# Kernel tuning notes

Measured on AMD Instinct MI355X. Metric: run time of the kernel, lower is better.

The kernel has to match this reference:

```python
import jax, jax.numpy as jnp
import numpy as np

H = 32  # hidden size, fixed by the source module


def setup_inputs() -> dict:
    key = jax.random.key(0)
    ks = jax.random.split(key, 11)
    B, T = 1024, 999
    s = 0.1  # weight init scale
    return {
        "input": jax.random.normal(ks[0], (B, T), jnp.float32),
        "W_ih1": jax.random.normal(ks[1], (4 * H, 1), jnp.float32) * s,
        "W_hh1": jax.random.normal(ks[2], (4 * H, H), jnp.float32) * s,
        "b_ih1": jax.random.normal(ks[3], (4 * H,), jnp.float32) * s,
        "b_hh1": jax.random.normal(ks[4], (4 * H,), jnp.float32) * s,
        "W_ih2": jax.random.normal(ks[5], (4 * H, H), jnp.float32) * s,
        "W_hh2": jax.random.normal(ks[6], (4 * H, H), jnp.float32) * s,
        "b_ih2": jax.random.normal(ks[7], (4 * H,), jnp.float32) * s,
        "b_hh2": jax.random.normal(ks[8], (4 * H,), jnp.float32) * s,
        "W_lin": jax.random.normal(ks[9], (1, H), jnp.float32) * s,
        "b_lin": jax.random.normal(ks[10], (1,), jnp.float32) * s,
        "future": 1000,
    }


def _lstm_cell(x, h, c, W_ih, W_hh, b_ih, b_hh):
    # PyTorch LSTMCell: gates = x@W_ih^T + b_ih + h@W_hh^T + b_hh, order i,f,g,o
    z = x @ W_ih.T + h @ W_hh.T + (b_ih + b_hh)
    i, f, g, o = jnp.split(z, 4, axis=-1)
    c_new = jax.nn.sigmoid(f) * c + jax.nn.sigmoid(i) * jnp.tanh(g)
    h_new = jax.nn.sigmoid(o) * jnp.tanh(c_new)
    return h_new, c_new


def reference(input, W_ih1, W_hh1, b_ih1, b_hh1, W_ih2, W_hh2, b_ih2, b_hh2,
              W_lin, b_lin, future):
    B = input.shape[0]
    dt = input.dtype
    z = jnp.zeros((B, H), dt)

    def step_tf(carry, x_t):  # teacher-forced phase, x_t: [B]
        h1, c1, h2, c2 = carry
        h1, c1 = _lstm_cell(x_t[:, None], h1, c1, W_ih1, W_hh1, b_ih1, b_hh1)
        h2, c2 = _lstm_cell(h1, h2, c2, W_ih2, W_hh2, b_ih2, b_hh2)
        out = h2 @ W_lin.T + b_lin  # [B,1]
        return (h1, c1, h2, c2), out[:, 0]

    carry, outs1 = jax.lax.scan(step_tf, (z, z, z, z), input.T)  # outs1: [T,B]

    def step_gen(carry, _):
        h1, c1, h2, c2, out = carry
        h1, c1 = _lstm_cell(out, h1, c1, W_ih1, W_hh1, b_ih1, b_hh1)
        h2, c2 = _lstm_cell(h1, h2, c2, W_ih2, W_hh2, b_ih2, b_hh2)
        out = h2 @ W_lin.T + b_lin
        return (h1, c1, h2, c2, out), out[:, 0]

    last_out = outs1[-1][:, None]
    _, outs2 = jax.lax.scan(step_gen, (*carry, last_out), None, length=future)

    return jnp.concatenate([outs1, outs2], axis=0).T  # [B, T+future]
```

## Files before the change

kernel.cpp:

```cpp
#include <hip/hip_runtime.h>

#define HH 32
#define LOG2E 1.44269504088896340736f
#define KCH 16

typedef float v2f __attribute__((ext_vector_type(2)));

#define DPPF(v, ctrl) \
    __int_as_float(__builtin_amdgcn_update_dpp(0, __float_as_int(v), (ctrl), 0xF, 0xF, true))
#define QP_B0 0x00
#define QP_B1 0x55
#define QP_B2 0xAA
#define QP_B3 0xFF
#define DPP_ROR4  0x124
#define DPP_ROR8  0x128
#define SWZ(v, pat) __int_as_float(__builtin_amdgcn_ds_swizzle(__float_as_int(v), (pat)))

__device__ __forceinline__ float hw_exp2(float x) {
    float r; asm("v_exp_f32 %0, %1" : "=v"(r) : "v"(x)); return r;
}
__device__ __forceinline__ float sigm_e(float z, float e) {
    return __builtin_amdgcn_rcpf(1.0f + hw_exp2(z * e));
}
__device__ __forceinline__ v2f pk_fma(v2f a, v2f b, v2f c) {
    return __builtin_elementwise_fma(a, b, c);
}
__device__ __forceinline__ void load_bc(const float* p, v2f* d) {
#pragma unroll
    for (int r = 0; r < 8; ++r) {
        float4 v = ((const float4*)p)[r];
        d[2*r]   = (v2f){v.x, v.y};
        d[2*r+1] = (v2f){v.z, v.w};
    }
}
__device__ __forceinline__ float out_reduce(float p) {
    p += DPPF(p, DPP_ROR4);
    p += DPPF(p, DPP_ROR8);
    p += SWZ(p, 0x401F);
    p += __shfl_xor(p, 32, 64);
    return p;
}

template<bool ACC>
__device__ __forceinline__ void dot2(const v2f* hv, const v2f* mA, const v2f* mB,
                                     v2f& P0, v2f& P1, v2f& P2, v2f& P3) {
    if (ACC) {
        P0 = pk_fma(hv[0], mA[0], P0); P1 = pk_fma(hv[1], mA[1], P1);
        P2 = pk_fma(hv[0], mB[0], P2); P3 = pk_fma(hv[1], mB[1], P3);
    } else {
        P0 = hv[0] * mA[0]; P1 = hv[1] * mA[1];
        P2 = hv[0] * mB[0]; P3 = hv[1] * mB[1];
    }
#pragma unroll
    for (int r = 2; r < 16; r += 2) {
        P0 = pk_fma(hv[r],   mA[r],   P0);
        P1 = pk_fma(hv[r+1], mA[r+1], P1);
        P2 = pk_fma(hv[r],   mB[r],   P2);
        P3 = pk_fma(hv[r+1], mB[r+1], P3);
    }
}

__device__ __forceinline__ void gate_hc(float zA, float zB, float es, float mm, float cc,
                                        float& cA, float& cB, float& hA, float& hB) {
    float acA = fmaf(mm, sigm_e(zA, es), cc);
    float acB = fmaf(mm, sigm_e(zB, es), cc);
    float iA = DPPF(acA, QP_B0), fA = DPPF(acA, QP_B1);
    float gA = DPPF(acA, QP_B2), oA = DPPF(acA, QP_B3);
    float iB = DPPF(acB, QP_B0), fB = DPPF(acB, QP_B1);
    float gB = DPPF(acB, QP_B2), oB = DPPF(acB, QP_B3);
    cA = fmaf(fA, cA, iA * gA);
    cB = fmaf(fB, cB, iB * gB);
    hA = oA * fmaf(2.0f, sigm_e(cA, -2.0f * LOG2E), -1.0f);
    hB = oB * fmaf(2.0f, sigm_e(cB, -2.0f * LOG2E), -1.0f);
}

__global__ __launch_bounds__(128, 2)
void lstm_seq_kernel(const float* __restrict__ input,
                     const float* __restrict__ W_ih1, const float* __restrict__ W_hh1,
                     const float* __restrict__ b_ih1, const float* __restrict__ b_hh1,
                     const float* __restrict__ W_ih2, const float* __restrict__ W_hh2,
                     const float* __restrict__ b_ih2, const float* __restrict__ b_hh2,
                     const float* __restrict__ W_lin, const float* __restrict__ b_lin,
                     float* __restrict__ out, int T, int total)
{
    const int b    = blockIdx.x;
    const int tid  = threadIdx.x;
    const int w    = tid >> 6;
    const int lane = tid & 63;
    const int q    = lane & 3;
    const int ch   = lane >> 2;
    const int rowA = (q << 5) | ch;
    const int rowB = (q << 5) | (ch + 16);

    __shared__ __align__(16) float ring[2 * KCH * HH];
    __shared__ __align__(16) float h1x[HH];
    __shared__ __align__(16) float h2s[HH];

    const bool  isg = (q == 2);
    const float es  = isg ? (-2.0f * LOG2E) : (-LOG2E);
    const float mm  = isg ? 2.0f : 1.0f;
    const float cc  = isg ? -1.0f : 0.0f;

    v2f m1A[16], m1B[16], m2A[16], m2B[16], wl[16];
    float wxA = 0.f, wxB = 0.f, bA, bB, wlA = 0.f, wlB = 0.f, blin;
    if (w == 0) {
        const v2f* pA = (const v2f*)(W_hh1 + rowA * HH);
        const v2f* pB = (const v2f*)(W_hh1 + rowB * HH);
        const v2f* wp = (const v2f*)W_lin;
#pragma unroll
        for (int r = 0; r < 16; ++r) { m1A[r] = pA[r]; m1B[r] = pB[r]; wl[r] = wp[r]; }
        wxA = W_ih1[rowA]; wxB = W_ih1[rowB];
        bA  = b_ih1[rowA] + b_hh1[rowA];
        bB  = b_ih1[rowB] + b_hh1[rowB];
    } else {
        const v2f* pA = (const v2f*)(W_ih2 + rowA * HH);
        const v2f* pB = (const v2f*)(W_ih2 + rowB * HH);
        const v2f* qA = (const v2f*)(W_hh2 + rowA * HH);
        const v2f* qB = (const v2f*)(W_hh2 + rowB * HH);
#pragma unroll
        for (int r = 0; r < 16; ++r) { m1A[r] = pA[r]; m1B[r] = pB[r];
                                       m2A[r] = qA[r]; m2B[r] = qB[r]; }
        bA  = b_ih2[rowA] + b_hh2[rowA];
        bB  = b_ih2[rowB] + b_hh2[rowB];
        wlA = W_lin[ch]; wlB = W_lin[ch + 16];
    }
    blin = b_lin[0];

    float cA = 0.f, cB = 0.f;
    v2f p0 = {0.f,0.f}, p1 = {0.f,0.f}, p2 = {0.f,0.f}, p3 = {0.f,0.f};

    const float* __restrict__ inp  = input + (size_t)b * T;
    float* __restrict__       outp = out   + (size_t)b * total;

    if (w == 0) {
        int t = 0;
        float xcur = inp[0];
        for (int cb = 0; t < T; ++cb) {
            float* buf = ring + (cb & 1) * (KCH * HH);
            int S = T - t; if (S > KCH) S = KCH;
            for (int s = 0; s < S; ++s, ++t) {
                float x = xcur;
                int tn = t + 1;
                xcur = inp[tn < T ? tn : 0];
                float z1A = fmaf(x, wxA, bA + (p0.x + p0.y) + (p1.x + p1.y));
                float z1B = fmaf(x, wxB, bB + (p2.x + p2.y) + (p3.x + p3.y));
                float hA, hB;
                gate_hc(z1A, z1B, es, mm, cc, cA, cB, hA, hB);
                float* slot = buf + s * HH;
                if (q == 0) { slot[ch] = hA; slot[ch + 16] = hB; }
                v2f hv[16]; load_bc(slot, hv);
                dot2<false>(hv, m1A, m1B, p0, p1, p2, p3);
            }
            __syncthreads();
        }
        __syncthreads();
    } else {
        __syncthreads();
        int t = 0;
        for (int cb = 0; t < T; ++cb) {
            const float* buf = ring + (cb & 1) * (KCH * HH);
            int S = T - t; if (S > KCH) S = KCH;
            for (int s = 0; s < S; ++s, ++t) {
                v2f hv[16]; load_bc(buf + s * HH, hv);
                dot2<true>(hv, m1A, m1B, p0, p1, p2, p3);
                float z2A = bA + (p0.x + p0.y) + (p1.x + p1.y);
                float z2B = bB + (p2.x + p2.y) + (p3.x + p3.y);
                float hA, hB;
                gate_hc(z2A, z2B, es, mm, cc, cA, cB, hA, hB);
                if (q == 0) { h2s[ch] = hA; h2s[ch + 16] = hB; }
                v2f gv[16]; load_bc(h2s, gv);
                dot2<false>(gv, m2A, m2B, p0, p1, p2, p3);
                float pr = fmaf(hA, wlA, hB * wlB);
                float ov = out_reduce(pr) + blin;
                if (lane == 0) outp[t] = ov;
            }
            __syncthreads();
        }
    }

    for (int t = T; t < total; ++t) {
        __syncthreads();
        if (w == 0) {
            v2f gv[16]; load_bc(h2s, gv);
            v2f oa = gv[0] * wl[0], ob = gv[1] * wl[1];
#pragma unroll
            for (int r = 2; r < 16; r += 2) { oa = pk_fma(gv[r],   wl[r],   oa);
                                              ob = pk_fma(gv[r+1], wl[r+1], ob); }
            float xo = (oa.x + oa.y) + (ob.x + ob.y) + blin;
            if (t > T && lane == 0) outp[t - 1] = xo;
            float z1A = fmaf(xo, wxA, bA + (p0.x + p0.y) + (p1.x + p1.y));
            float z1B = fmaf(xo, wxB, bB + (p2.x + p2.y) + (p3.x + p3.y));
            float hA, hB;
            gate_hc(z1A, z1B, es, mm, cc, cA, cB, hA, hB);
            if (q == 0) { h1x[ch] = hA; h1x[ch + 16] = hB; }
        } else {
            v2f gv[16]; load_bc(h2s, gv);
            dot2<false>(gv, m2A, m2B, p0, p1, p2, p3);
        }
        __syncthreads();
        if (w == 0) {
            v2f hv[16]; load_bc(h1x, hv);
            dot2<false>(hv, m1A, m1B, p0, p1, p2, p3);
        } else {
            v2f hv[16]; load_bc(h1x, hv);
            dot2<true>(hv, m1A, m1B, p0, p1, p2, p3);
            float z2A = bA + (p0.x + p0.y) + (p1.x + p1.y);
            float z2B = bB + (p2.x + p2.y) + (p3.x + p3.y);
            float hA, hB;
            gate_hc(z2A, z2B, es, mm, cc, cA, cB, hA, hB);
            if (q == 0) { h2s[ch] = hA; h2s[ch + 16] = hB; }
        }
    }
    __syncthreads();
    if (w == 0) {
        v2f gv[16]; load_bc(h2s, gv);
        v2f oa = gv[0] * wl[0], ob = gv[1] * wl[1];
#pragma unroll
        for (int r = 2; r < 16; r += 2) { oa = pk_fma(gv[r],   wl[r],   oa);
                                          ob = pk_fma(gv[r+1], wl[r+1], ob); }
        if (lane == 0) outp[total - 1] = (oa.x + oa.y) + (ob.x + ob.y) + blin;
    }
}

extern "C" void kernel_launch(void* const* d_in, const int* in_sizes, int n_in,
                              void* d_out, int out_size, void* d_ws, size_t ws_size,
                              hipStream_t stream) {
    const int B = 1024;
    const int T = in_sizes[0] / B;
    const int total = out_size / B;

    lstm_seq_kernel<<<dim3(B), dim3(128), 0, stream>>>(
        (const float*)d_in[0],
        (const float*)d_in[1], (const float*)d_in[2],
        (const float*)d_in[3], (const float*)d_in[4],
        (const float*)d_in[5], (const float*)d_in[6],
        (const float*)d_in[7], (const float*)d_in[8],
        (const float*)d_in[9], (const float*)d_in[10],
        (float*)d_out, T, total);
}
```

Before: 1.205 ms.

## Split each LSTM cell across two waves and pipeline layers with per-step barriers

Each block now uses four waves: two per LSTM layer, each wave owning 16 hidden channels, replacing one wave per layer that handled 32 channels each. The teacher-forced phase drops the decoupled 16-step ring buffer and instead runs layer 1 one step ahead of layer 2 in lockstep, with double-buffered hidden states in shared memory and a block barrier every step. The output projection is reduced across the two layer-2 waves through shared memory. The aim is to halve the per-wave dot-product and gate work on the serial critical path, at the cost of a __syncthreads on every timestep and twice the threads per block.

```diff
diff --git a/kernel.cpp b/kernel.cpp
--- a/kernel.cpp
+++ b/kernel.cpp
@@ -2,7 +2,6 @@
 
 #define HH 32
 #define LOG2E 1.44269504088896340736f
-#define KCH 16
 
 typedef float v2f __attribute__((ext_vector_type(2)));
 
@@ -25,14 +24,7 @@
 __device__ __forceinline__ v2f pk_fma(v2f a, v2f b, v2f c) {
     return __builtin_elementwise_fma(a, b, c);
 }
-__device__ __forceinline__ void load_bc(const float* p, v2f* d) {
-#pragma unroll
-    for (int r = 0; r < 8; ++r) {
-        float4 v = ((const float4*)p)[r];
-        d[2*r]   = (v2f){v.x, v.y};
-        d[2*r+1] = (v2f){v.z, v.w};
-    }
-}
+
 __device__ __forceinline__ float out_reduce(float p) {
     p += DPPF(p, DPP_ROR4);
     p += DPPF(p, DPP_ROR8);
@@ -41,40 +33,51 @@
     return p;
 }
 
-template<bool ACC>
-__device__ __forceinline__ void dot2(const v2f* hv, const v2f* mA, const v2f* mB,
-                                     v2f& P0, v2f& P1, v2f& P2, v2f& P3) {
-    if (ACC) {
-        P0 = pk_fma(hv[0], mA[0], P0); P1 = pk_fma(hv[1], mA[1], P1);
-        P2 = pk_fma(hv[0], mB[0], P2); P3 = pk_fma(hv[1], mB[1], P3);
-    } else {
-        P0 = hv[0] * mA[0]; P1 = hv[1] * mA[1];
-        P2 = hv[0] * mB[0]; P3 = hv[1] * mB[1];
-    }
+__device__ __forceinline__ float dotv(const float* va, const v2f* m) {
+    const float4* pa = (const float4*)va;
+    float4 a = pa[0], b = pa[1];
+    v2f s0 = (v2f){a.x,a.y} * m[0], s1 = (v2f){a.z,a.w} * m[1];
+    v2f s2 = (v2f){b.x,b.y} * m[2], s3 = (v2f){b.z,b.w} * m[3];
 #pragma unroll
-    for (int r = 2; r < 16; r += 2) {
-        P0 = pk_fma(hv[r],   mA[r],   P0);
-        P1 = pk_fma(hv[r+1], mA[r+1], P1);
-        P2 = pk_fma(hv[r],   mB[r],   P2);
-        P3 = pk_fma(hv[r+1], mB[r+1], P3);
-    }
-}
-
-__device__ __forceinline__ void gate_hc(float zA, float zB, float es, float mm, float cc,
-                                        float& cA, float& cB, float& hA, float& hB) {
-    float acA = fmaf(mm, sigm_e(zA, es), cc);
-    float acB = fmaf(mm, sigm_e(zB, es), cc);
-    float iA = DPPF(acA, QP_B0), fA = DPPF(acA, QP_B1);
-    float gA = DPPF(acA, QP_B2), oA = DPPF(acA, QP_B3);
-    float iB = DPPF(acB, QP_B0), fB = DPPF(acB, QP_B1);
-    float gB = DPPF(acB, QP_B2), oB = DPPF(acB, QP_B3);
-    cA = fmaf(fA, cA, iA * gA);
-    cB = fmaf(fB, cB, iB * gB);
-    hA = oA * fmaf(2.0f, sigm_e(cA, -2.0f * LOG2E), -1.0f);
-    hB = oB * fmaf(2.0f, sigm_e(cB, -2.0f * LOG2E), -1.0f);
-}
-
-__global__ __launch_bounds__(128, 2)
+    for (int rr = 2; rr < 8; rr += 2) {
+        float4 c = pa[rr], d = pa[rr+1];
+        s0 = pk_fma((v2f){c.x,c.y}, m[2*rr],   s0);
+        s1 = pk_fma((v2f){c.z,c.w}, m[2*rr+1], s1);
+        s2 = pk_fma((v2f){d.x,d.y}, m[2*rr+2], s2);
+        s3 = pk_fma((v2f){d.z,d.w}, m[2*rr+3], s3);
+    }
+    v2f t = (s0 + s1) + (s2 + s3);
+    return t.x + t.y;
+}
+
+__device__ __forceinline__ float dotv2f(const float* va, const v2f* ma,
+                                        const float* vb, const v2f* mb) {
+    const float4* pa = (const float4*)va;
+    const float4* pb = (const float4*)vb;
+    float4 a = pa[0], b = pb[0];
+    v2f s0 = (v2f){a.x,a.y} * ma[0], s1 = (v2f){a.z,a.w} * ma[1];
+    v2f s2 = (v2f){b.x,b.y} * mb[0], s3 = (v2f){b.z,b.w} * mb[1];
+#pragma unroll
+    for (int rr = 1; rr < 8; ++rr) {
+        float4 c = pa[rr], d = pb[rr];
+        s0 = pk_fma((v2f){c.x,c.y}, ma[2*rr],   s0);
+        s1 = pk_fma((v2f){c.z,c.w}, ma[2*rr+1], s1);
+        s2 = pk_fma((v2f){d.x,d.y}, mb[2*rr],   s2);
+        s3 = pk_fma((v2f){d.z,d.w}, mb[2*rr+1], s3);
+    }
+    v2f t = (s0 + s1) + (s2 + s3);
+    return t.x + t.y;
+}
+
+__device__ __forceinline__ float gate1(float z, float es, float mm, float cc, float& c) {
+    float ac = fmaf(mm, sigm_e(z, es), cc);
+    float gi = DPPF(ac, QP_B0), gf = DPPF(ac, QP_B1);
+    float gg = DPPF(ac, QP_B2), go = DPPF(ac, QP_B3);
+    c = fmaf(gf, c, gi * gg);
+    return go * fmaf(2.0f, sigm_e(c, -2.0f * LOG2E), -1.0f);
+}
+
+__global__ __launch_bounds__(256, 4)
 void lstm_seq_kernel(const float* __restrict__ input,
                      const float* __restrict__ W_ih1, const float* __restrict__ W_hh1,
                      const float* __restrict__ b_ih1, const float* __restrict__ b_hh1,
@@ -85,140 +88,105 @@
 {
     const int b    = blockIdx.x;
     const int tid  = threadIdx.x;
-    const int w    = tid >> 6;
+    const int wv   = tid >> 6;
     const int lane = tid & 63;
+    const int cell = wv >> 1;
+    const int half = wv & 1;
     const int q    = lane & 3;
-    const int ch   = lane >> 2;
-    const int rowA = (q << 5) | ch;
-    const int rowB = (q << 5) | (ch + 16);
-
-    __shared__ __align__(16) float ring[2 * KCH * HH];
-    __shared__ __align__(16) float h1x[HH];
-    __shared__ __align__(16) float h2s[HH];
+    const int ch   = (lane >> 2) + (half << 4);
+    const int row  = (q << 5) | ch;
+
+    __shared__ __align__(16) float h1buf[2][HH];
+    __shared__ __align__(16) float h2buf[2][HH];
+    __shared__ float outP[2][2];
+
+    if (tid < HH) {
+        h1buf[0][tid] = 0.f; h1buf[1][tid] = 0.f;
+        h2buf[0][tid] = 0.f; h2buf[1][tid] = 0.f;
+    }
+    if (tid < 4) outP[tid >> 1][tid & 1] = 0.f;
 
     const bool  isg = (q == 2);
     const float es  = isg ? (-2.0f * LOG2E) : (-LOG2E);
     const float mm  = isg ? 2.0f : 1.0f;
     const float cc  = isg ? -1.0f : 0.0f;
 
-    v2f m1A[16], m1B[16], m2A[16], m2B[16], wl[16];
-    float wxA = 0.f, wxB = 0.f, bA, bB, wlA = 0.f, wlB = 0.f, blin;
-    if (w == 0) {
-        const v2f* pA = (const v2f*)(W_hh1 + rowA * HH);
-        const v2f* pB = (const v2f*)(W_hh1 + rowB * HH);
-        const v2f* wp = (const v2f*)W_lin;
+    const v2f* m1p = (const v2f*)((cell == 0 ? W_hh1 : W_ih2) + row * HH);
+    const v2f* m2p = (cell == 0) ? (const v2f*)W_lin
+                                 : (const v2f*)(W_hh2 + row * HH);
+    v2f m1[16], m2[16];
 #pragma unroll
-        for (int r = 0; r < 16; ++r) { m1A[r] = pA[r]; m1B[r] = pB[r]; wl[r] = wp[r]; }
-        wxA = W_ih1[rowA]; wxB = W_ih1[rowB];
-        bA  = b_ih1[rowA] + b_hh1[rowA];
-        bB  = b_ih1[rowB] + b_hh1[rowB];
-    } else {
-        const v2f* pA = (const v2f*)(W_ih2 + rowA * HH);
-        const v2f* pB = (const v2f*)(W_ih2 + rowB * HH);
-        const v2f* qA = (const v2f*)(W_hh2 + rowA * HH);
-        const v2f* qB = (const v2f*)(W_hh2 + rowB * HH);
-#pragma unroll
-        for (int r = 0; r < 16; ++r) { m1A[r] = pA[r]; m1B[r] = pB[r];
-                                       m2A[r] = qA[r]; m2B[r] = qB[r]; }
-        bA  = b_ih2[rowA] + b_hh2[rowA];
-        bB  = b_ih2[rowB] + b_hh2[rowB];
-        wlA = W_lin[ch]; wlB = W_lin[ch + 16];
-    }
-    blin = b_lin[0];
-
-    float cA = 0.f, cB = 0.f;
-    v2f p0 = {0.f,0.f}, p1 = {0.f,0.f}, p2 = {0.f,0.f}, p3 = {0.f,0.f};
+    for (int r = 0; r < 16; ++r) { m1[r] = m1p[r]; m2[r] = m2p[r]; }
+
+    const float wx  = W_ih1[row];
+    const float bb  = (cell == 0) ? (b_ih1[row] + b_hh1[row])
+                                  : (b_ih2[row] + b_hh2[row]);
+    const float wlc = W_lin[ch];
+    const float blin = b_lin[0];
+
+    float cst = 0.f;
+    float pAR = 0.f;
 
     const float* __restrict__ inp  = input + (size_t)b * T;
     float* __restrict__       outp = out   + (size_t)b * total;
 
-    if (w == 0) {
-        int t = 0;
-        float xcur = inp[0];
-        for (int cb = 0; t < T; ++cb) {
-            float* buf = ring + (cb & 1) * (KCH * HH);
-            int S = T - t; if (S > KCH) S = KCH;
-            for (int s = 0; s < S; ++s, ++t) {
+    float xcur = inp[0];
+    for (int t = 0; t <= T; ++t) {
+        __syncthreads();
+        if (cell == 0) {
+            if (t < T) {
+                float pd = dotv(h1buf[(t + 1) & 1], m1);
                 float x = xcur;
                 int tn = t + 1;
                 xcur = inp[tn < T ? tn : 0];
-                float z1A = fmaf(x, wxA, bA + (p0.x + p0.y) + (p1.x + p1.y));
-                float z1B = fmaf(x, wxB, bB + (p2.x + p2.y) + (p3.x + p3.y));
-                float hA, hB;
-                gate_hc(z1A, z1B, es, mm, cc, cA, cB, hA, hB);
-                float* slot = buf + s * HH;
-                if (q == 0) { slot[ch] = hA; slot[ch + 16] = hB; }
-                v2f hv[16]; load_bc(slot, hv);
-                dot2<false>(hv, m1A, m1B, p0, p1, p2, p3);
+                float z1 = fmaf(x, wx, bb + pd);
+                float h = gate1(z1, es, mm, cc, cst);
+                if (q == 0) h1buf[t & 1][ch] = h;
+            } else {
+                pAR = dotv(h1buf[(T - 1) & 1], m1);
             }
-            __syncthreads();
+        } else {
+            if (t >= 1) {
+                float zd = dotv2f(h1buf[(t - 1) & 1], m1, h2buf[t & 1], m2);
+                float z2 = bb + zd;
+                float h = gate1(z2, es, mm, cc, cst);
+                if (q == 0) h2buf[(t - 1) & 1][ch] = h;
+                float po = out_reduce(h * wlc);
+                if (lane == 0) outP[(t - 1) & 1][half] = po;
+            }
+            if (t >= 2 && wv == 2 && lane == 0)
+                outp[t - 2] = outP[t & 1][0] + outP[t & 1][1] + blin;
+        }
+    }
+
+    float* h2x = h2buf[(T - 1) & 1];
+    float* h1x = h1buf[0];
+    float sAR = 0.f;
+
+    for (int t = T; t < total; ++t) {
+        __syncthreads();
+        if (cell == 0) {
+            float xo = dotv(h2x, m2) + blin;
+            if (wv == 0 && lane == 0) outp[t - 1] = xo;
+            float z1 = fmaf(xo, wx, bb + pAR);
+            float h = gate1(z1, es, mm, cc, cst);
+            if (q == 0) h1x[ch] = h;
+        } else {
+            sAR = dotv(h2x, m2);
         }
         __syncthreads();
-    } else {
-        __syncthreads();
-        int t = 0;
-        for (int cb = 0; t < T; ++cb) {
-            const float* buf = ring + (cb & 1) * (KCH * HH);
-            int S = T - t; if (S > KCH) S = KCH;
-            for (int s = 0; s < S; ++s, ++t) {
-                v2f hv[16]; load_bc(buf + s * HH, hv);
-                dot2<true>(hv, m1A, m1B, p0, p1, p2, p3);
-                float z2A = bA + (p0.x + p0.y) + (p1.x + p1.y);
-                float z2B = bB + (p2.x + p2.y) + (p3.x + p3.y);
-                float hA, hB;
-                gate_hc(z2A, z2B, es, mm, cc, cA, cB, hA, hB);
-                if (q == 0) { h2s[ch] = hA; h2s[ch + 16] = hB; }
-                v2f gv[16]; load_bc(h2s, gv);
-                dot2<false>(gv, m2A, m2B, p0, p1, p2, p3);
-                float pr = fmaf(hA, wlA, hB * wlB);
-                float ov = out_reduce(pr) + blin;
-                if (lane == 0) outp[t] = ov;
-            }
-            __syncthreads();
+        if (cell == 0) {
+            pAR = dotv(h1x, m1);
+        } else {
+            float z2 = bb + sAR + dotv(h1x, m1);
+            float h = gate1(z2, es, mm, cc, cst);
+            if (q == 0) h2x[ch] = h;
         }
     }
-
-    for (int t = T; t < total; ++t) {
-        __syncthreads();
-        if (w == 0) {
-            v2f gv[16]; load_bc(h2s, gv);
-            v2f oa = gv[0] * wl[0], ob = gv[1] * wl[1];
-#pragma unroll
-            for (int r = 2; r < 16; r += 2) { oa = pk_fma(gv[r],   wl[r],   oa);
-                                              ob = pk_fma(gv[r+1], wl[r+1], ob); }
-            float xo = (oa.x + oa.y) + (ob.x + ob.y) + blin;
-            if (t > T && lane == 0) outp[t - 1] = xo;
-            float z1A = fmaf(xo, wxA, bA + (p0.x + p0.y) + (p1.x + p1.y));
-            float z1B = fmaf(xo, wxB, bB + (p2.x + p2.y) + (p3.x + p3.y));
-            float hA, hB;
-            gate_hc(z1A, z1B, es, mm, cc, cA, cB, hA, hB);
-            if (q == 0) { h1x[ch] = hA; h1x[ch + 16] = hB; }
-        } else {
-            v2f gv[16]; load_bc(h2s, gv);
-            dot2<false>(gv, m2A, m2B, p0, p1, p2, p3);
-        }
-        __syncthreads();
-        if (w == 0) {
-            v2f hv[16]; load_bc(h1x, hv);
-            dot2<false>(hv, m1A, m1B, p0, p1, p2, p3);
-        } else {
-            v2f hv[16]; load_bc(h1x, hv);
-            dot2<true>(hv, m1A, m1B, p0, p1, p2, p3);
-            float z2A = bA + (p0.x + p0.y) + (p1.x + p1.y);
-            float z2B = bB + (p2.x + p2.y) + (p3.x + p3.y);
-            float hA, hB;
-            gate_hc(z2A, z2B, es, mm, cc, cA, cB, hA, hB);
-            if (q == 0) { h2s[ch] = hA; h2s[ch + 16] = hB; }
-        }
-    }
     __syncthreads();
-    if (w == 0) {
-        v2f gv[16]; load_bc(h2s, gv);
-        v2f oa = gv[0] * wl[0], ob = gv[1] * wl[1];
-#pragma unroll
-        for (int r = 2; r < 16; r += 2) { oa = pk_fma(gv[r],   wl[r],   oa);
-                                          ob = pk_fma(gv[r+1], wl[r+1], ob); }
-        if (lane == 0) outp[total - 1] = (oa.x + oa.y) + (ob.x + ob.y) + blin;
+    if (wv == 0) {
+        float xo = dotv(h2x, m2) + blin;
+        if (lane == 0) outp[total - 1] = xo;
     }
 }
 
@@ -229,7 +197,7 @@
     const int T = in_sizes[0] / B;
     const int total = out_size / B;
 
-    lstm_seq_kernel<<<dim3(B), dim3(128), 0, stream>>>(
+    lstm_seq_kernel<<<dim3(B), dim3(256), 0, stream>>>(
         (const float*)d_in[0],
         (const float*)d_in[1], (const float*)d_in[2],
         (const float*)d_in[3], (const float*)d_in[4],
```

After: 1.403 ms. 1.16x slower.

## Run autoregressive phase on a single wavefront without block barriers

Applied to the files above, without the earlier changes.

After the teacher-forced phase, wave 1 saves its layer-2 cell state to shared memory and exits, and wave 0 runs both LSTM layers alone for the generation steps. This removes the two __syncthreads per step and the cross-wave handoff. W_ih2 and W_hh2 are loaded into registers and W_hh1 is moved to padded shared memory to limit register pressure. The cost is serialising work that two waves previously shared, and adding LDS reads for the W_hh1 dot product.

```diff
diff --git a/kernel.cpp b/kernel.cpp
--- a/kernel.cpp
+++ b/kernel.cpp
@@ -3,6 +3,7 @@
 #define HH 32
 #define LOG2E 1.44269504088896340736f
 #define KCH 16
+#define WPAD 36
 
 typedef float v2f __attribute__((ext_vector_type(2)));
 
@@ -95,6 +96,8 @@
     __shared__ __align__(16) float ring[2 * KCH * HH];
     __shared__ __align__(16) float h1x[HH];
     __shared__ __align__(16) float h2s[HH];
+    __shared__ __align__(16) float c2x[HH];
+    __shared__ __align__(16) float whh1l[128 * WPAD];
 
     const bool  isg = (q == 2);
     const float es  = isg ? (-2.0f * LOG2E) : (-LOG2E);
@@ -174,45 +177,68 @@
                 float ov = out_reduce(pr) + blin;
                 if (lane == 0) outp[t] = ov;
             }
+            if (t >= T && q == 0) { c2x[ch] = cA; c2x[ch + 16] = cB; }
             __syncthreads();
         }
-    }
+        return;
+    }
+
+#pragma unroll
+    for (int k = 0; k < 16; ++k) {
+        ((v2f*)(whh1l + rowA * WPAD))[k] = m1A[k];
+        ((v2f*)(whh1l + rowB * WPAD))[k] = m1B[k];
+    }
+    float c2A = c2x[ch], c2B = c2x[ch + 16];
+    v2f i2A[16], i2B[16], w2A[16], w2B[16];
+    {
+        const v2f* a1 = (const v2f*)(W_ih2 + rowA * HH);
+        const v2f* a2 = (const v2f*)(W_ih2 + rowB * HH);
+        const v2f* a3 = (const v2f*)(W_hh2 + rowA * HH);
+        const v2f* a4 = (const v2f*)(W_hh2 + rowB * HH);
+#pragma unroll
+        for (int r = 0; r < 16; ++r) { i2A[r] = a1[r]; i2B[r] = a2[r];
+                                       w2A[r] = a3[r]; w2B[r] = a4[r]; }
+    }
+    const float b2A = b_ih2[rowA] + b_hh2[rowA];
+    const float b2B = b_ih2[rowB] + b_hh2[rowB];
 
     for (int t = T; t < total; ++t) {
-        __syncthreads();
-        if (w == 0) {
-            v2f gv[16]; load_bc(h2s, gv);
-            v2f oa = gv[0] * wl[0], ob = gv[1] * wl[1];
-#pragma unroll
-            for (int r = 2; r < 16; r += 2) { oa = pk_fma(gv[r],   wl[r],   oa);
-                                              ob = pk_fma(gv[r+1], wl[r+1], ob); }
-            float xo = (oa.x + oa.y) + (ob.x + ob.y) + blin;
-            if (t > T && lane == 0) outp[t - 1] = xo;
-            float z1A = fmaf(xo, wxA, bA + (p0.x + p0.y) + (p1.x + p1.y));
-            float z1B = fmaf(xo, wxB, bB + (p2.x + p2.y) + (p3.x + p3.y));
-            float hA, hB;
-            gate_hc(z1A, z1B, es, mm, cc, cA, cB, hA, hB);
-            if (q == 0) { h1x[ch] = hA; h1x[ch + 16] = hB; }
-        } else {
-            v2f gv[16]; load_bc(h2s, gv);
-            dot2<false>(gv, m2A, m2B, p0, p1, p2, p3);
+        v2f gv[16]; load_bc(h2s, gv);
+        v2f oa = gv[0] * wl[0], ob = gv[1] * wl[1];
+#pragma unroll
+        for (int r = 2; r < 16; r += 2) { oa = pk_fma(gv[r],   wl[r],   oa);
+                                          ob = pk_fma(gv[r+1], wl[r+1], ob); }
+        float xo = (oa.x + oa.y) + (ob.x + ob.y) + blin;
+        if (lane == 0) outp[t - 1] = xo;
+        v2f s0, s1, s2, s3;
+        dot2<false>(gv, w2A, w2B, s0, s1, s2, s3);
+        float z1A = fmaf(xo, wxA, bA + (p0.x + p0.y) + (p1.x + p1.y));
+        float z1B = fmaf(xo, wxB, bB + (p2.x + p2.y) + (p3.x + p3.y));
+        float hA, hB;
+        gate_hc(z1A, z1B, es, mm, cc, cA, cB, hA, hB);
+        if (q == 0) { h1x[ch] = hA; h1x[ch + 16] = hB; }
+        v2f hv[16]; load_bc(h1x, hv);
+        dot2<true>(hv, i2A, i2B, s0, s1, s2, s3);
+        float z2A = b2A + (s0.x + s0.y) + (s1.x + s1.y);
+        float z2B = b2B + (s2.x + s2.y) + (s3.x + s3.y);
+        float h2a, h2b;
+        gate_hc(z2A, z2B, es, mm, cc, c2A, c2B, h2a, h2b);
+        if (q == 0) { h2s[ch] = h2a; h2s[ch + 16] = h2b; }
+        const float4* wrA = (const float4*)(whh1l + rowA * WPAD);
+        const float4* wrB = (const float4*)(whh1l + rowB * WPAD);
+        float4 wa = wrA[0], wb = wrB[0];
+        p0 = (v2f){wa.x, wa.y} * hv[0]; p1 = (v2f){wa.z, wa.w} * hv[1];
+        p2 = (v2f){wb.x, wb.y} * hv[0]; p3 = (v2f){wb.z, wb.w} * hv[1];
+#pragma unroll
+        for (int k = 1; k < 8; ++k) {
+            float4 ua = wrA[k], ub = wrB[k];
+            p0 = pk_fma((v2f){ua.x, ua.y}, hv[2*k],   p0);
+            p1 = pk_fma((v2f){ua.z, ua.w}, hv[2*k+1], p1);
+            p2 = pk_fma((v2f){ub.x, ub.y}, hv[2*k],   p2);
+            p3 = pk_fma((v2f){ub.z, ub.w}, hv[2*k+1], p3);
         }
-        __syncthreads();
-        if (w == 0) {
-            v2f hv[16]; load_bc(h1x, hv);
-            dot2<false>(hv, m1A, m1B, p0, p1, p2, p3);
-        } else {
-            v2f hv[16]; load_bc(h1x, hv);
-            dot2<true>(hv, m1A, m1B, p0, p1, p2, p3);
-            float z2A = bA + (p0.x + p0.y) + (p1.x + p1.y);
-            float z2B = bB + (p2.x + p2.y) + (p3.x + p3.y);
-            float hA, hB;
-            gate_hc(z2A, z2B, es, mm, cc, cA, cB, hA, hB);
-            if (q == 0) { h2s[ch] = hA; h2s[ch + 16] = hB; }
-        }
-    }
-    __syncthreads();
-    if (w == 0) {
+    }
+    {
         v2f gv[16]; load_bc(h2s, gv);
         v2f oa = gv[0] * wl[0], ob = gv[1] * wl[1];
 #pragma unroll
```

Result: slower. 1.495 ms (+24.1%).

## Move layer-2 input projection to the layer-1 wave in the teacher-forced phase

Applied to the files above, without the earlier changes.

During the teacher-forced phase, wave 0 now computes the layer-2 input projection W_ih2·h1 right after producing h1. It passes the resulting gate pre-activations to wave 1 through a larger shared-memory ring, instead of passing h1 itself. Wave 1's per-step critical path shrinks to only the recurrent W_hh2 product, which balances work across the two pipelined waves. The cost is extra register pressure in wave 0, which now holds both W_hh1 and W_ih2. The ring also grows from 32 to 128 floats per step, and the partial-sum adds are rewritten as packed vector adds.

```diff
diff --git a/kernel.cpp b/kernel.cpp
--- a/kernel.cpp
+++ b/kernel.cpp
@@ -91,8 +91,10 @@
     const int ch   = lane >> 2;
     const int rowA = (q << 5) | ch;
     const int rowB = (q << 5) | (ch + 16);
-
-    __shared__ __align__(16) float ring[2 * KCH * HH];
+    const int zidx = (q << 4) | ch;
+
+    __shared__ __align__(16) float zring[2 * KCH * 128];
+    __shared__ __align__(16) float h1self[HH];
     __shared__ __align__(16) float h1x[HH];
     __shared__ __align__(16) float h2s[HH];
 
@@ -101,14 +103,17 @@
     const float mm  = isg ? 2.0f : 1.0f;
     const float cc  = isg ? -1.0f : 0.0f;
 
-    v2f m1A[16], m1B[16], m2A[16], m2B[16], wl[16];
-    float wxA = 0.f, wxB = 0.f, bA, bB, wlA = 0.f, wlB = 0.f, blin;
+    v2f m1A[16], m1B[16], m2A[16], m2B[16];
+    float wxA = 0.f, wxB = 0.f, bA, bB, blin;
+    const float wlA = W_lin[ch], wlB = W_lin[ch + 16];
     if (w == 0) {
         const v2f* pA = (const v2f*)(W_hh1 + rowA * HH);
         const v2f* pB = (const v2f*)(W_hh1 + rowB * HH);
-        const v2f* wp = (const v2f*)W_lin;
-#pragma unroll
-        for (int r = 0; r < 16; ++r) { m1A[r] = pA[r]; m1B[r] = pB[r]; wl[r] = wp[r]; }
+        const v2f* qA = (const v2f*)(W_ih2 + rowA * HH);
+        const v2f* qB = (const v2f*)(W_ih2 + rowB * HH);
+#pragma unroll
+        for (int r = 0; r < 16; ++r) { m1A[r] = pA[r]; m1B[r] = pB[r];
+                                       m2A[r] = qA[r]; m2B[r] = qB[r]; }
         wxA = W_ih1[rowA]; wxB = W_ih1[rowB];
         bA  = b_ih1[rowA] + b_hh1[rowA];
         bB  = b_ih1[rowB] + b_hh1[rowB];
@@ -122,7 +127,6 @@
                                        m2A[r] = qA[r]; m2B[r] = qB[r]; }
         bA  = b_ih2[rowA] + b_hh2[rowA];
         bB  = b_ih2[rowB] + b_hh2[rowB];
-        wlA = W_lin[ch]; wlB = W_lin[ch + 16];
     }
     blin = b_lin[0];
 
@@ -136,20 +140,26 @@
         int t = 0;
         float xcur = inp[0];
         for (int cb = 0; t < T; ++cb) {
-            float* buf = ring + (cb & 1) * (KCH * HH);
+            float* zbuf = zring + (cb & 1) * (KCH * 128);
             int S = T - t; if (S > KCH) S = KCH;
             for (int s = 0; s < S; ++s, ++t) {
                 float x = xcur;
                 int tn = t + 1;
                 xcur = inp[tn < T ? tn : 0];
-                float z1A = fmaf(x, wxA, bA + (p0.x + p0.y) + (p1.x + p1.y));
-                float z1B = fmaf(x, wxB, bB + (p2.x + p2.y) + (p3.x + p3.y));
+                v2f tA = p0 + p1, tB = p2 + p3;
+                float z1A = fmaf(x, wxA, bA + tA.x + tA.y);
+                float z1B = fmaf(x, wxB, bB + tB.x + tB.y);
                 float hA, hB;
                 gate_hc(z1A, z1B, es, mm, cc, cA, cB, hA, hB);
-                float* slot = buf + s * HH;
-                if (q == 0) { slot[ch] = hA; slot[ch + 16] = hB; }
-                v2f hv[16]; load_bc(slot, hv);
+                if (q == 0) { h1self[ch] = hA; h1self[ch + 16] = hB; }
+                v2f hv[16]; load_bc(h1self, hv);
                 dot2<false>(hv, m1A, m1B, p0, p1, p2, p3);
+                v2f s0, s1, s2, s3;
+                dot2<false>(hv, m2A, m2B, s0, s1, s2, s3);
+                v2f uA = s0 + s1, uB = s2 + s3;
+                float* zs = zbuf + s * 128;
+                zs[zidx]      = uA.x + uA.y;
+                zs[zidx + 64] = uB.x + uB.y;
             }
             __syncthreads();
         }
@@ -158,13 +168,14 @@
         __syncthreads();
         int t = 0;
         for (int cb = 0; t < T; ++cb) {
-            const float* buf = ring + (cb & 1) * (KCH * HH);
+            const float* zbuf = zring + (cb & 1) * (KCH * 128);
             int S = T - t; if (S > KCH) S = KCH;
             for (int s = 0; s < S; ++s, ++t) {
-                v2f hv[16]; load_bc(buf + s * HH, hv);
-                dot2<true>(hv, m1A, m1B, p0, p1, p2, p3);
-                float z2A = bA + (p0.x + p0.y) + (p1.x + p1.y);
-                float z2B = bB + (p2.x + p2.y) + (p3.x + p3.y);
+                const float* zs = zbuf + s * 128;
+                float zihA = zs[zidx], zihB = zs[zidx + 64];
+                v2f tA = p0 + p1, tB = p2 + p3;
+                float z2A = bA + zihA + tA.x + tA.y;
+                float z2B = bB + zihB + tB.x + tB.y;
                 float hA, hB;
                 gate_hc(z2A, z2B, es, mm, cc, cA, cB, hA, hB);
                 if (q == 0) { h2s[ch] = hA; h2s[ch + 16] = hB; }
@@ -178,6 +189,12 @@
         }
     }
 
+    v2f wl[16];
+    if (w == 0) {
+        const v2f* wp = (const v2f*)W_lin;
+#pragma unroll
+        for (int r = 0; r < 16; ++r) wl[r] = wp[r];
+    }
     for (int t = T; t < total; ++t) {
         __syncthreads();
         if (w == 0) {
@@ -188,8 +205,9 @@
                                               ob = pk_fma(gv[r+1], wl[r+1], ob); }
             float xo = (oa.x + oa.y) + (ob.x + ob.y) + blin;
             if (t > T && lane == 0) outp[t - 1] = xo;
-            float z1A = fmaf(xo, wxA, bA + (p0.x + p0.y) + (p1.x + p1.y));
-            float z1B = fmaf(xo, wxB, bB + (p2.x + p2.y) + (p3.x + p3.y));
+            v2f tA = p0 + p1, tB = p2 + p3;
+            float z1A = fmaf(xo, wxA, bA + tA.x + tA.y);
+            float z1B = fmaf(xo, wxB, bB + tB.x + tB.y);
             float hA, hB;
             gate_hc(z1A, z1B, es, mm, cc, cA, cB, hA, hB);
             if (q == 0) { h1x[ch] = hA; h1x[ch + 16] = hB; }
@@ -204,8 +222,9 @@
         } else {
             v2f hv[16]; load_bc(h1x, hv);
             dot2<true>(hv, m1A, m1B, p0, p1, p2, p3);
-            float z2A = bA + (p0.x + p0.y) + (p1.x + p1.y);
-            float z2B = bB + (p2.x + p2.y) + (p3.x + p3.y);
+            v2f tA = p0 + p1, tB = p2 + p3;
+            float z2A = bA + tA.x + tA.y;
+            float z2B = bB + tB.x + tB.y;
             float hA, hB;
             gate_hc(z2A, z2B, es, mm, cc, cA, cB, hA, hB);
             if (q == 0) { h2s[ch] = hA; h2s[ch + 16] = hB; }
```

After: 1.154 ms (median of 2 runs). 4.2% less time.
